# Optimization experiments

Hardware: AMD Instinct MI355X
Metric: run time of the kernel (lower is better)

## Reference

```python
import jax, jax.numpy as jnp
import numpy as np

N_NODES = 50000
N_REL = 8
N_EDGES = 400000  # per relation
D_IN = 256
D_OUT = 256


def setup_inputs() -> dict:
    key = jax.random.key(0)
    k1, k2, k3, k4, k5 = jax.random.split(key, 5)
    gain = np.sqrt(2.0)  # relu gain used by xavier init in the module
    x = jax.random.normal(k1, (N_NODES, D_IN), dtype=jnp.float32)
    weight = jax.random.normal(k2, (N_REL, D_IN, D_OUT), dtype=jnp.float32) * (gain / np.sqrt(D_IN + D_OUT))
    h_bias = jnp.zeros((D_OUT,), dtype=jnp.float32)
    loop_weight = jax.random.normal(k3, (D_IN, D_OUT), dtype=jnp.float32) * (gain / np.sqrt(D_IN + D_OUT))
    src_idx = jax.random.randint(k4, (N_REL, N_EDGES), 0, N_NODES, dtype=jnp.int32)
    dst_idx = jax.random.randint(k5, (N_REL, N_EDGES), 0, N_NODES, dtype=jnp.int32)
    return {"x": x, "weight": weight, "h_bias": h_bias, "loop_weight": loop_weight,
            "src_idx": src_idx, "dst_idx": dst_idx}


def reference(x, weight, h_bias, loop_weight, src_idx, dst_idx):
    # x: [N, D_in]; weight: [R, D_in, D_out]; src/dst_idx: [R, E]
    n = x.shape[0]
    out = jnp.zeros((n, weight.shape[-1]), dtype=x.dtype)
    # Loop over the small fixed set of relations (structurally distinct weights).
    for r in range(weight.shape[0]):
        h = x @ weight[r]                                   # [N, D_out] transform-first (in<=out path of GraphConv)
        msg = h[src_idx[r]]                                 # [E, D_out] gather
        agg = jax.ops.segment_sum(msg, dst_idx[r], num_segments=n)  # [N, D_out] scatter-add
        deg = jax.ops.segment_sum(jnp.ones((dst_idx.shape[1],), dtype=x.dtype),
                                  dst_idx[r], num_segments=n)
        out = out + agg / jnp.clip(deg, 1.0)[:, None]       # norm='right': divide by in-degree (clamped at 1)
    out = out + x @ loop_weight + h_bias                    # self-loop + bias
    return jax.nn.relu(out)                                  # activation; dropout(p=0) is identity
```

## Files before the change

### kernel.cpp

```cpp
#include <hip/hip_runtime.h>
#include <hip/hip_bf16.h>

#define NN 50000
#define NPAD 50048
#define NR 8
#define NE 400000
#define PCAP 16
#define OCAP 16
#define CHUNK 2048
#define CPB 196
#define NRANGE 6250
#define XBLK 12500
#define TBLK 144

typedef __attribute__((ext_vector_type(8))) short short8v;
typedef __attribute__((ext_vector_type(4))) float f32x4;
typedef __attribute__((ext_vector_type(2))) unsigned int uint2v;

static __device__ __forceinline__ ushort f2b(float f) {
  union { float f; unsigned u; } v; v.f = f;
  unsigned u = v.u;
  unsigned r = (u + 0x7fffu + ((u >> 16) & 1u)) >> 16;
  return (ushort)r;
}
static __device__ __forceinline__ float b2f(ushort u) {
  union { unsigned u; float f; } v; v.u = ((unsigned)u) << 16;
  return v.f;
}


__global__ __launch_bounds__(256) void k_prep(const float* __restrict__ x,
                                              const float* __restrict__ w,
                                              const float* __restrict__ lw,
                                              ushort* __restrict__ xb,
                                              ushort* __restrict__ wb,
                                              const int* __restrict__ src,
                                              const int* __restrict__ dst,
                                              int* __restrict__ cnt,
                                              ushort* __restrict__ csrp,
                                              ushort* __restrict__ ovf) {
  __shared__ ushort tile[64][66];
  int b = blockIdx.x;
  if (b < XBLK) {
    int i = b * 256 + threadIdx.x;
    float4 v = ((const float4*)x)[i];
    ushort4 o;
    o.x = f2b(v.x); o.y = f2b(v.y); o.z = f2b(v.z); o.w = f2b(v.w);
    ((ushort4*)xb)[i] = o;
    return;
  }
  if (b < XBLK + TBLK) {
    int tb = b - XBLK;
    int s = tb >> 4, t16 = tb & 15;
    int kt = (t16 >> 2) * 64, nt2 = (t16 & 3) * 64;
    const float* srcw = (s < 8) ? (w + (size_t)s * 65536) : lw;
    int t = threadIdx.x;
    #pragma unroll
    for (int i = 0; i < 16; ++i) {
      int flat = i * 256 + t;
      int kk = flat >> 6, nn = flat & 63;
      tile[kk][nn] = f2b(srcw[(size_t)(kt + kk) * 256 + nt2 + nn]);
    }
    __syncthreads();
    #pragma unroll
    for (int i = 0; i < 16; ++i) {
      int flat = i * 256 + t;
      int nn2 = flat >> 6, kk2 = flat & 63;
      wb[(size_t)s * 65536 + (size_t)(nt2 + nn2) * 256 + kt + kk2] = tile[kk2][nn2];
    }
    return;
  }
  int xcd = b & 7;
  int rc = (b - XBLK - TBLK) >> 3;
  int r = rc / CPB;
  int c = rc - r * CPB;
  int nlo = xcd * NRANGE, nhi = nlo + NRANGE;
  const int* dr = dst + (size_t)r * NE;
  const int* sr = src + (size_t)r * NE;
  int e0 = c * CHUNK + threadIdx.x * 4;
  #pragma unroll
  for (int u = 0; u < CHUNK / 1024; ++u) {
    int e = e0 + u * 1024;
    if (e + 3 < NE) {
      int4 d4 = *(const int4*)(dr + e);
      int4 s4 = *(const int4*)(sr + e);
      #pragma unroll
      for (int k = 0; k < 4; ++k) {
        int d = (k == 0) ? d4.x : (k == 1) ? d4.y : (k == 2) ? d4.z : d4.w;
        int s = (k == 0) ? s4.x : (k == 1) ? s4.y : (k == 2) ? s4.z : s4.w;
        if (d >= nlo && d < nhi) {
          int slot = atomicAdd(&cnt[r * NN + d], 1);
          if (slot < PCAP)
            csrp[((size_t)r * NN + d) * PCAP + slot] = (ushort)s;
          else if (slot < PCAP + OCAP)
            ovf[((size_t)r * NN + d) * OCAP + (slot - PCAP)] = (ushort)s;
        }
      }
    } else {
      for (int k = 0; k < 4; ++k) {
        int e2 = e + k;
        if (e2 < NE) {
          int d = dr[e2];
          if (d >= nlo && d < nhi) {
            int slot = atomicAdd(&cnt[r * NN + d], 1);
            if (slot < PCAP)
              csrp[((size_t)r * NN + d) * PCAP + slot] = (ushort)sr[e2];
            else if (slot < PCAP + OCAP)
              ovf[((size_t)r * NN + d) * OCAP + (slot - PCAP)] = (ushort)sr[e2];
          }
        }
      }
    }
  }
}


__global__ __launch_bounds__(256) void k_agg(const ushort* __restrict__ xb,
                                             const ushort* __restrict__ csrp,
                                             const ushort* __restrict__ ovf,
                                             const int* __restrict__ cnt,
                                             ushort* __restrict__ xa,
                                             long strideR, int r0) {
  int wid = threadIdx.x >> 6, lane = threadIdx.x & 63;
  int n = blockIdx.x * 4 + wid;
  int r = r0 + blockIdx.y;
  if (n >= NN) return;
  int dg = cnt[r * NN + n];
  int m = min(dg, PCAP + OCAP);
  int m1 = min(m, PCAP);
  const ushort* lst = csrp + ((size_t)r * NN + n) * PCAP;
  float a0 = 0.f, a1 = 0.f, a2 = 0.f, a3 = 0.f;
  int j = 0;
  for (; j + 3 < m1; j += 4) {
    int s0 = lst[j], s1 = lst[j + 1], s2 = lst[j + 2], s3 = lst[j + 3];
    ushort4 v0 = *(const ushort4*)(xb + (size_t)s0 * 256 + lane * 4);
    ushort4 v1 = *(const ushort4*)(xb + (size_t)s1 * 256 + lane * 4);
    ushort4 v2 = *(const ushort4*)(xb + (size_t)s2 * 256 + lane * 4);
    ushort4 v3 = *(const ushort4*)(xb + (size_t)s3 * 256 + lane * 4);
    a0 += (b2f(v0.x) + b2f(v1.x)) + (b2f(v2.x) + b2f(v3.x));
    a1 += (b2f(v0.y) + b2f(v1.y)) + (b2f(v2.y) + b2f(v3.y));
    a2 += (b2f(v0.z) + b2f(v1.z)) + (b2f(v2.z) + b2f(v3.z));
    a3 += (b2f(v0.w) + b2f(v1.w)) + (b2f(v2.w) + b2f(v3.w));
  }
  for (; j < m1; ++j) {
    ushort4 v0 = *(const ushort4*)(xb + (size_t)lst[j] * 256 + lane * 4);
    a0 += b2f(v0.x); a1 += b2f(v0.y); a2 += b2f(v0.z); a3 += b2f(v0.w);
  }
  if (m > PCAP) {
    const ushort* lst2 = ovf + ((size_t)r * NN + n) * OCAP;
    for (int j2 = 0; j2 < m - PCAP; ++j2) {
      ushort4 v0 = *(const ushort4*)(xb + (size_t)lst2[j2] * 256 + lane * 4);
      a0 += b2f(v0.x); a1 += b2f(v0.y); a2 += b2f(v0.z); a3 += b2f(v0.w);
    }
  }
  float inv = 1.f / (float)max(dg, 1);
  unsigned w0 = ((unsigned)f2b(a0 * inv)) | (((unsigned)f2b(a1 * inv)) << 16);
  unsigned w1 = ((unsigned)f2b(a2 * inv)) | (((unsigned)f2b(a3 * inv)) << 16);
  uint2v o; o[0] = w0; o[1] = w1;
  __builtin_nontemporal_store(o, (uint2v*)(xa + (size_t)(r - r0) * strideR +
                                           (size_t)n * 256 + lane * 4));
}


#define BK 64

__global__ __launch_bounds__(512, 4) void k_gemm(
    const ushort* __restrict__ xa, long strideR, int nseg,
    const ushort* __restrict__ xb8, const ushort* __restrict__ wb, int wseg0,
    const float* __restrict__ bias, float* __restrict__ out, int first, int final_) {
  __shared__ ushort As[2][128 * BK];
  __shared__ ushort Bs[256 * BK];
  int t = threadIdx.x;
  int lane = t & 63, wid = t >> 6;
  int wm = wid >> 2, wn = wid & 3;
  int i0 = blockIdx.x * 128;
  const int NT = nseg * 4;

  f32x4 acc[4][4];
  #pragma unroll
  for (int a = 0; a < 4; ++a)
    #pragma unroll
    for (int b = 0; b < 4; ++b) acc[a][b] = (f32x4){0.f, 0.f, 0.f, 0.f};

#define STAGE_A(stp, buf) do {                                                  \
    int s_ = (stp) >> 2; int kt_ = ((stp) & 3) * 64;                            \
    const ushort* A_ = (wseg0 + s_ < 8) ? (xa + (size_t)s_ * strideR) : xb8;    \
    _Pragma("unroll")                                                           \
    for (int it = 0; it < 2; ++it) {                                            \
      int c = it * 512 + t; int row = c >> 3, sg = c & 7;                       \
      int sgg = sg ^ (row & 7);                                                 \
      const ushort* ga = A_ + (size_t)(i0 + row) * 256 + kt_ + sgg * 8;         \
      __builtin_amdgcn_global_load_lds(                                         \
          (const __attribute__((address_space(1))) unsigned int*)ga,            \
          (__attribute__((address_space(3))) unsigned int*)(As[buf] + c * 8),   \
          16, 0, 0);                                                            \
    } } while (0)

#define STAGE_B(stp) do {                                                       \
    int s_ = (stp) >> 2; int kt_ = ((stp) & 3) * 64;                            \
    const ushort* W_ = wb + (size_t)(wseg0 + s_) * 65536;                       \
    _Pragma("unroll")                                                           \
    for (int it = 0; it < 4; ++it) {                                            \
      int c = it * 512 + t; int row = c >> 3, sg = c & 7;                       \
      int sgg = sg ^ (row & 7);                                                 \
      const ushort* gb = W_ + (size_t)row * 256 + kt_ + sgg * 8;                \
      __builtin_amdgcn_global_load_lds(                                         \
          (const __attribute__((address_space(1))) unsigned int*)gb,            \
          (__attribute__((address_space(3))) unsigned int*)(Bs + c * 8),        \
          16, 0, 0);                                                            \
    } } while (0)

  STAGE_A(0, 0);
  int cur = 0;
  #pragma unroll 1
  for (int st = 0; st < NT; ++st) {
    __builtin_amdgcn_s_barrier();
    STAGE_B(st);
    if (st + 1 < NT) {
      STAGE_A(st + 1, cur ^ 1);
      asm volatile("s_waitcnt vmcnt(2)" ::: "memory");
    } else {
      asm volatile("s_waitcnt vmcnt(0)" ::: "memory");
    }
    __builtin_amdgcn_sched_barrier(0);
    __builtin_amdgcn_s_barrier();
    __builtin_amdgcn_sched_barrier(0);
    const ushort* Ac = As[cur];
    #pragma unroll
    for (int kk = 0; kk < 2; ++kk) {
      int ko = kk * 32 + (lane >> 4) * 8;
      int kb = ko * 2;
      short8v a_frag[4], b_frag[4];
      #pragma unroll
      for (int mi = 0; mi < 4; ++mi) {
        int row = wm * 64 + mi * 16 + (lane & 15);
        int ba = row * 128 + (kb ^ ((row & 7) << 4));
        a_frag[mi] = *(const short8v*)((const char*)Ac + ba);
      }
      #pragma unroll
      for (int ni = 0; ni < 4; ++ni) {
        int row = wn * 64 + ni * 16 + (lane & 15);
        int ba = row * 128 + (kb ^ ((row & 7) << 4));
        b_frag[ni] = *(const short8v*)((const char*)Bs + ba);
      }
      #pragma unroll
      for (int mi = 0; mi < 4; ++mi)
        #pragma unroll
        for (int ni = 0; ni < 4; ++ni)
          acc[mi][ni] = __builtin_amdgcn_mfma_f32_16x16x32_bf16(
              a_frag[mi], b_frag[ni], acc[mi][ni], 0, 0, 0);
    }
    cur ^= 1;
  }
#undef STAGE_A
#undef STAGE_B

  #pragma unroll
  for (int mi = 0; mi < 4; ++mi) {
    int rbase = i0 + wm * 64 + mi * 16 + ((lane >> 4) << 2);
    #pragma unroll
    for (int ni = 0; ni < 4; ++ni) {
      int col = wn * 64 + ni * 16 + (lane & 15);
      float bv = final_ ? bias[col] : 0.f;
      #pragma unroll
      for (int rg = 0; rg < 4; ++rg) {
        int gm = rbase + rg;
        if (gm < NN) {
          size_t o = (size_t)gm * 256 + col;
          float v = acc[mi][ni][rg];
          if (!first) v += out[o];
          if (final_) v = fmaxf(v + bv, 0.f);
          out[o] = v;
        }
      }
    }
  }
}


extern "C" void kernel_launch(void* const* d_in, const int* in_sizes, int n_in,
                              void* d_out, int out_size, void* d_ws, size_t ws_size,
                              hipStream_t stream) {
  const float* x = (const float*)d_in[0];
  const float* w = (const float*)d_in[1];
  const float* bias = (const float*)d_in[2];
  const float* lw = (const float*)d_in[3];
  const int* src = (const int*)d_in[4];
  const int* dst = (const int*)d_in[5];
  float* out = (float*)d_out;

  char* ws = (char*)d_ws;
  size_t off = 0;
  auto carve = [&](size_t bytes) {
    size_t o = off;
    off = (off + bytes + 255) & ~(size_t)255;
    return o;
  };
  int* cnt = (int*)(ws + carve((size_t)NR * NN * 4));
  ushort* csrp = (ushort*)(ws + carve((size_t)NR * NN * PCAP * 2));
  ushort* ovf = (ushort*)(ws + carve((size_t)NR * NN * OCAP * 2));
  ushort* wb = (ushort*)(ws + carve((size_t)9 * 65536 * 2));
  ushort* xb = (ushort*)(ws + carve((size_t)NPAD * 256 * 2));
  size_t base_bytes = off;
  ushort* xa = (ushort*)(ws + off);
  const size_t segb = (size_t)NPAD * 256 * 2;
  long strideR = (long)NPAD * 256;

  (void)hipMemsetAsync(cnt, 0, (size_t)NR * NN * 4, stream);
  k_prep<<<XBLK + TBLK + 8 * CPB * NR, 256, 0, stream>>>(x, w, lw, xb, wb,
                                                         src, dst, cnt, csrp, ovf);

  dim3 gemm_grid(NPAD / 128);
  if (ws_size >= base_bytes + 8 * segb) {
    k_agg<<<dim3((NN + 3) / 4, 8), 256, 0, stream>>>(xb, csrp, ovf, cnt, xa, strideR, 0);
    k_gemm<<<gemm_grid, 512, 0, stream>>>(xa, strideR, 9, xb, wb, 0, bias, out, 1, 1);
  } else if (ws_size >= base_bytes + 4 * segb) {
    k_agg<<<dim3((NN + 3) / 4, 4), 256, 0, stream>>>(xb, csrp, ovf, cnt, xa, strideR, 0);
    k_gemm<<<gemm_grid, 512, 0, stream>>>(xa, strideR, 4, xb, wb, 0, bias, out, 1, 0);
    k_agg<<<dim3((NN + 3) / 4, 4), 256, 0, stream>>>(xb, csrp, ovf, cnt, xa, strideR, 4);
    k_gemm<<<gemm_grid, 512, 0, stream>>>(xa, strideR, 5, xb, wb, 4, bias, out, 0, 1);
  } else {
    for (int r = 0; r < 8; ++r) {
      k_agg<<<dim3((NN + 3) / 4, 1), 256, 0, stream>>>(xb, csrp, ovf, cnt, xa, strideR, r);
      k_gemm<<<gemm_grid, 512, 0, stream>>>(xa, strideR, 1, xb, wb, r, bias, out,
                                            (r == 0) ? 1 : 0, 0);
    }
    k_gemm<<<gemm_grid, 512, 0, stream>>>(xa, strideR, 1, xb, wb, 8, bias, out, 0, 1);
  }
  (void)in_sizes; (void)n_in; (void)out_size;
}
```

Before: 451.3 us.

## Bucket edges by destination range before scattering into per-node CSR

Replaces the edge-binning pass, in which every block rescanned its edge chunk eight times and kept only one destination range, with a two-phase scheme. First, blocks partition edges into per-relation, per-destination-range queues, using shared-memory counts and one global atomic per bucket, and pack (dst,src) into 32 bits. A new scatter kernel then reads each queue and performs the per-node slot atomics into the CSR arrays. This avoids the eightfold redundant index reads, at the cost of an extra launch and queue traffic. The queues alias the xa buffer, and the QCAP truncation assumes the buckets stay near uniform.

```diff
diff --git a/kernel.cpp b/kernel.cpp
--- a/kernel.cpp
+++ b/kernel.cpp
@@ -7,11 +7,12 @@
 #define NE 400000
 #define PCAP 16
 #define OCAP 16
-#define CHUNK 2048
-#define CPB 196
 #define NRANGE 6250
+#define FCH 8192
+#define FBLK 392
 #define XBLK 12500
 #define TBLK 144
+#define QCAP 56320
 
 typedef __attribute__((ext_vector_type(8))) short short8v;
 typedef __attribute__((ext_vector_type(4))) float f32x4;
@@ -36,25 +37,59 @@
                                               ushort* __restrict__ wb,
                                               const int* __restrict__ src,
                                               const int* __restrict__ dst,
-                                              int* __restrict__ cnt,
-                                              ushort* __restrict__ csrp,
-                                              ushort* __restrict__ ovf) {
+                                              int* __restrict__ qcnt,
+                                              unsigned* __restrict__ q) {
   __shared__ ushort tile[64][66];
+  __shared__ int lcnt[8];
+  __shared__ int lbase[8];
   int b = blockIdx.x;
+  int t = threadIdx.x;
+  if (b < FBLK) {
+    int r = b / 49, c = b % 49;
+    const int* dr = dst + (size_t)r * NE;
+    const int* sr = src + (size_t)r * NE;
+    int e0 = c * FCH;
+    if (t < 8) lcnt[t] = 0;
+    __syncthreads();
+    #pragma unroll 4
+    for (int it = 0; it < FCH / 256; ++it) {
+      int e = e0 + it * 256 + t;
+      if (e < NE) atomicAdd(&lcnt[dr[e] / NRANGE], 1);
+    }
+    __syncthreads();
+    if (t < 8) {
+      lbase[t] = atomicAdd(&qcnt[r * 8 + t], lcnt[t]);
+      lcnt[t] = 0;
+    }
+    __syncthreads();
+    #pragma unroll 4
+    for (int it = 0; it < FCH / 256; ++it) {
+      int e = e0 + it * 256 + t;
+      if (e < NE) {
+        int d = dr[e], s = sr[e];
+        int g = d / NRANGE;
+        int p = atomicAdd(&lcnt[g], 1);
+        int pos = lbase[g] + p;
+        if (pos < QCAP)
+          q[((size_t)r * 8 + g) * QCAP + pos] = ((unsigned)d << 16) | (unsigned)s;
+      }
+    }
+    return;
+  }
+  b -= FBLK;
   if (b < XBLK) {
-    int i = b * 256 + threadIdx.x;
+    int i = b * 256 + t;
     float4 v = ((const float4*)x)[i];
     ushort4 o;
     o.x = f2b(v.x); o.y = f2b(v.y); o.z = f2b(v.z); o.w = f2b(v.w);
     ((ushort4*)xb)[i] = o;
     return;
   }
-  if (b < XBLK + TBLK) {
-    int tb = b - XBLK;
-    int s = tb >> 4, t16 = tb & 15;
+  b -= XBLK;
+  {
+    int s = b >> 4, t16 = b & 15;
     int kt = (t16 >> 2) * 64, nt2 = (t16 & 3) * 64;
     const float* srcw = (s < 8) ? (w + (size_t)s * 65536) : lw;
-    int t = threadIdx.x;
     #pragma unroll
     for (int i = 0; i < 16; ++i) {
       int flat = i * 256 + t;
@@ -68,49 +103,30 @@
       int nn2 = flat >> 6, kk2 = flat & 63;
       wb[(size_t)s * 65536 + (size_t)(nt2 + nn2) * 256 + kt + kk2] = tile[kk2][nn2];
     }
-    return;
-  }
-  int xcd = b & 7;
-  int rc = (b - XBLK - TBLK) >> 3;
-  int r = rc / CPB;
-  int c = rc - r * CPB;
-  int nlo = xcd * NRANGE, nhi = nlo + NRANGE;
-  const int* dr = dst + (size_t)r * NE;
-  const int* sr = src + (size_t)r * NE;
-  int e0 = c * CHUNK + threadIdx.x * 4;
-  #pragma unroll
-  for (int u = 0; u < CHUNK / 1024; ++u) {
-    int e = e0 + u * 1024;
-    if (e + 3 < NE) {
-      int4 d4 = *(const int4*)(dr + e);
-      int4 s4 = *(const int4*)(sr + e);
-      #pragma unroll
-      for (int k = 0; k < 4; ++k) {
-        int d = (k == 0) ? d4.x : (k == 1) ? d4.y : (k == 2) ? d4.z : d4.w;
-        int s = (k == 0) ? s4.x : (k == 1) ? s4.y : (k == 2) ? s4.z : s4.w;
-        if (d >= nlo && d < nhi) {
-          int slot = atomicAdd(&cnt[r * NN + d], 1);
-          if (slot < PCAP)
-            csrp[((size_t)r * NN + d) * PCAP + slot] = (ushort)s;
-          else if (slot < PCAP + OCAP)
-            ovf[((size_t)r * NN + d) * OCAP + (slot - PCAP)] = (ushort)s;
-        }
-      }
-    } else {
-      for (int k = 0; k < 4; ++k) {
-        int e2 = e + k;
-        if (e2 < NE) {
-          int d = dr[e2];
-          if (d >= nlo && d < nhi) {
-            int slot = atomicAdd(&cnt[r * NN + d], 1);
-            if (slot < PCAP)
-              csrp[((size_t)r * NN + d) * PCAP + slot] = (ushort)sr[e2];
-            else if (slot < PCAP + OCAP)
-              ovf[((size_t)r * NN + d) * OCAP + (slot - PCAP)] = (ushort)sr[e2];
-          }
-        }
-      }
-    }
+  }
+}
+
+
+__global__ __launch_bounds__(256) void k_scat(const unsigned* __restrict__ q,
+                                              const int* __restrict__ qcnt,
+                                              int* __restrict__ cnt,
+                                              ushort* __restrict__ csrp,
+                                              ushort* __restrict__ ovf) {
+  int g = blockIdx.x & 7;
+  int idx = blockIdx.x >> 3;
+  int r = idx & 7, part = idx >> 3;
+  int total = min(qcnt[r * 8 + g], QCAP);
+  int span = (total + 7) / 8;
+  int start = part * span, end = min(total, start + span);
+  const unsigned* myq = q + ((size_t)r * 8 + g) * QCAP;
+  for (int e = start + (int)threadIdx.x; e < end; e += 256) {
+    unsigned v = myq[e];
+    int d = v >> 16, s = v & 0xFFFF;
+    int slot = atomicAdd(&cnt[r * NN + d], 1);
+    if (slot < PCAP)
+      csrp[((size_t)r * NN + d) * PCAP + slot] = (ushort)s;
+    else if (slot < PCAP + OCAP)
+      ovf[((size_t)r * NN + d) * OCAP + (slot - PCAP)] = (ushort)s;
   }
 }
 
@@ -297,18 +313,21 @@
     return o;
   };
   int* cnt = (int*)(ws + carve((size_t)NR * NN * 4));
+  int* qcnt = (int*)(ws + carve((size_t)64 * 4));
   ushort* csrp = (ushort*)(ws + carve((size_t)NR * NN * PCAP * 2));
   ushort* ovf = (ushort*)(ws + carve((size_t)NR * NN * OCAP * 2));
   ushort* wb = (ushort*)(ws + carve((size_t)9 * 65536 * 2));
   ushort* xb = (ushort*)(ws + carve((size_t)NPAD * 256 * 2));
   size_t base_bytes = off;
   ushort* xa = (ushort*)(ws + off);
+  unsigned* q = (unsigned*)xa;
   const size_t segb = (size_t)NPAD * 256 * 2;
   long strideR = (long)NPAD * 256;
 
-  (void)hipMemsetAsync(cnt, 0, (size_t)NR * NN * 4, stream);
-  k_prep<<<XBLK + TBLK + 8 * CPB * NR, 256, 0, stream>>>(x, w, lw, xb, wb,
-                                                         src, dst, cnt, csrp, ovf);
+  (void)hipMemsetAsync(cnt, 0, (size_t)NR * NN * 4 + 512, stream);
+  k_prep<<<FBLK + XBLK + TBLK, 256, 0, stream>>>(x, w, lw, xb, wb,
+                                                 src, dst, qcnt, q);
+  k_scat<<<512, 256, 0, stream>>>(q, qcnt, cnt, csrp, ovf);
 
   dim3 gemm_grid(NPAD / 128);
   if (ws_size >= base_bytes + 8 * segb) {
```

New measurement: 565.8 us. 25.4% more time.
